# Optimization experiments

Hardware: AMD Instinct MI355X
Metric: run time of the kernel (lower is better)

Reference implementation:

```python
import jax, jax.numpy as jnp
import numpy as np

COMMITMENT_COST = 0.25


def setup_inputs() -> dict:
    key = jax.random.key(0)
    k1, k2 = jax.random.split(key)
    x = jax.random.normal(k1, (65536, 256), dtype=jnp.float32)
    codebook = jax.random.normal(k2, (1024, 256), dtype=jnp.float32)
    return {"x": x, "codebook": codebook}


def reference(x, codebook):
    # Flatten to [N, D] (already 2D here).
    flat = x.reshape(-1, codebook.shape[1])
    # Squared euclidean distances [N, K]; argmin matches torch.cdist argmin.
    x2 = jnp.sum(flat * flat, axis=1, keepdims=True)          # [N, 1]
    c2 = jnp.sum(codebook * codebook, axis=1)                  # [K]
    d2 = x2 - 2.0 * (flat @ codebook.T) + c2[None, :]          # [N, K]
    encoding_indices = jnp.argmin(d2, axis=1)                  # [N]
    quantized = codebook[encoding_indices]                     # [N, D]
    # VQ loss + commitment loss
    vq_loss = jnp.mean((jax.lax.stop_gradient(quantized) - flat) ** 2)
    commitment_loss = jnp.mean((quantized - jax.lax.stop_gradient(flat)) ** 2)
    quantization_loss = vq_loss + COMMITMENT_COST * commitment_loss
    # Straight-through estimator
    quantized_st = flat + jax.lax.stop_gradient(quantized - flat)
    quantized_st = quantized_st.reshape(x.shape)
    return quantized_st, quantization_loss, encoding_indices
```

## Files before the change

### kernel.cpp

```cpp
#include <hip/hip_runtime.h>

#define NROWS 65536
#define DDIM  256
#define KCODES 1024
#define MARGIN 0.05f
#define TIE_WINDOW 8.0e-5
#define FLAGCAP 8192

typedef __attribute__((ext_vector_type(8))) short bf16x8;
typedef __attribute__((ext_vector_type(4))) float f32x4;

union F4 { float4 v; float f[4]; };

__device__ __forceinline__ unsigned bf16rne(float f) {
    unsigned u = __float_as_uint(f);
    return (u + 0x7fffu + ((u >> 16) & 1u)) >> 16;
}
__device__ __forceinline__ float bf16tof(unsigned h) {
    return __uint_as_float(h << 16);
}

__global__ __launch_bounds__(64) void c2_kernel(const float* __restrict__ cb,
                                                float* __restrict__ c2f,
                                                double* __restrict__ c2d,
                                                int* __restrict__ cnt) {
    const int c = blockIdx.x, lane = threadIdx.x;
    if (c == 0 && lane == 0) cnt[0] = 0;
    F4 v; v.v = reinterpret_cast<const float4*>(cb + (size_t)c * DDIM)[lane];
    double s = (double)v.f[0] * v.f[0] + (double)v.f[1] * v.f[1]
             + (double)v.f[2] * v.f[2] + (double)v.f[3] * v.f[3];
    #pragma unroll
    for (int off = 32; off; off >>= 1) s += __shfl_xor(s, off);
    if (lane == 0) { c2d[c] = s; c2f[c] = (float)s; }
}

__global__ __launch_bounds__(256) void prep_frags(const float* __restrict__ cb,
                                                  unsigned short* __restrict__ fh,
                                                  unsigned short* __restrict__ fl) {
    int t = blockIdx.x * 256 + threadIdx.x;
    int j0   = (t & 1) * 4;
    int lane = (t >> 1) & 63;
    int ks   = (t >> 7) & 7;
    int ntg  = t >> 10;
    int c = ntg * 16 + (lane & 15);
    int k = ks * 32 + (lane >> 4) * 8 + j0;
    F4 v; v.v = *reinterpret_cast<const float4*>(cb + (size_t)c * DDIM + k);
    unsigned h0 = bf16rne(v.f[0]), h1 = bf16rne(v.f[1]),
             h2 = bf16rne(v.f[2]), h3 = bf16rne(v.f[3]);
    unsigned l0 = bf16rne(v.f[0] - bf16tof(h0)), l1 = bf16rne(v.f[1] - bf16tof(h1)),
             l2 = bf16rne(v.f[2] - bf16tof(h2)), l3 = bf16rne(v.f[3] - bf16tof(h3));
    unsigned* ph = reinterpret_cast<unsigned*>(fh + (size_t)t * 4);
    unsigned* pl = reinterpret_cast<unsigned*>(fl + (size_t)t * 4);
    ph[0] = h0 | (h1 << 16); ph[1] = h2 | (h3 << 16);
    pl[0] = l0 | (l1 << 16); pl[1] = l2 | (l3 << 16);
}

__global__ __launch_bounds__(512) void vqmfma(const float* __restrict__ x,
                                              const unsigned short* __restrict__ fbh,
                                              const unsigned short* __restrict__ fbl,
                                              const float* __restrict__ c2f,
                                              float* __restrict__ out_idx,
                                              int* __restrict__ flaglist,
                                              int* __restrict__ cnt,
                                              float* __restrict__ rowsq) {
    __shared__ bf16x8 lds_ah[1024];
    __shared__ bf16x8 lds_al[1024];
    __shared__ float  lds_c2[KCODES];
    __shared__ float  m_b1[256]; __shared__ float m_b2[256]; __shared__ int m_i1[256];
    __shared__ float  x2s[32];

    const int tid  = threadIdx.x;
    const int w    = tid >> 6;
    const int lane = tid & 63;
    const int row0 = blockIdx.x * 32;

    #pragma unroll
    for (int q = 0; q < 2; q++) lds_c2[q * 512 + tid] = c2f[q * 512 + tid];

    {
        const float4* gx = reinterpret_cast<const float4*>(x + (size_t)row0 * DDIM);
        unsigned* pah = reinterpret_cast<unsigned*>(lds_ah);
        unsigned* pal = reinterpret_cast<unsigned*>(lds_al);
        #pragma unroll
        for (int jj = 0; jj < 4; jj++) {
            int flat4 = jj * 512 + tid;
            int r = flat4 >> 6;
            int k = (flat4 & 63) * 4;
            F4 v; v.v = gx[flat4];
            float sq = v.f[0]*v.f[0] + v.f[1]*v.f[1] + v.f[2]*v.f[2] + v.f[3]*v.f[3];
            #pragma unroll
            for (int off = 32; off; off >>= 1) sq += __shfl_xor(sq, off);
            if (lane == 0) x2s[r] = sq;
            int rt = r >> 4, row = r & 15;
            int ks = k >> 5, gg = (k >> 3) & 3, j0 = k & 7;
            int laneS = gg * 16 + row;
            int u32i = ((((rt * 8 + ks) * 64 + laneS) * 8 + j0) >> 1);
            unsigned h0 = bf16rne(v.f[0]), h1 = bf16rne(v.f[1]),
                     h2 = bf16rne(v.f[2]), h3 = bf16rne(v.f[3]);
            pah[u32i]     = h0 | (h1 << 16);
            pah[u32i + 1] = h2 | (h3 << 16);
            unsigned l0 = bf16rne(v.f[0] - bf16tof(h0)), l1 = bf16rne(v.f[1] - bf16tof(h1)),
                     l2 = bf16rne(v.f[2] - bf16tof(h2)), l3 = bf16rne(v.f[3] - bf16tof(h3));
            pal[u32i]     = l0 | (l1 << 16);
            pal[u32i + 1] = l2 | (l3 << 16);
        }
    }
    __syncthreads();

    float bestv[8], secv[8]; int besti[8];
    #pragma unroll
    for (int e = 0; e < 8; e++) { bestv[e] = 1e30f; secv[e] = 1e30f; besti[e] = 0; }

    const bf16x8* Bh = reinterpret_cast<const bf16x8*>(fbh);
    const bf16x8* Bl = reinterpret_cast<const bf16x8*>(fbl);

    for (int cc = 0; cc < KCODES; cc += 256) {
        f32x4 acc[2][2];
        #pragma unroll
        for (int rt = 0; rt < 2; rt++)
            #pragma unroll
            for (int nt = 0; nt < 2; nt++) acc[rt][nt] = (f32x4){0.f, 0.f, 0.f, 0.f};

        const int ntg0 = (cc >> 4) + w * 2;
        const bf16x8* b0h = Bh + (size_t)(ntg0 * 8) * 64 + lane;
        const bf16x8* b0l = Bl + (size_t)(ntg0 * 8) * 64 + lane;
        const bf16x8* b1h = b0h + 8 * 64;
        const bf16x8* b1l = b0l + 8 * 64;
        const bf16x8* a0  = &lds_ah[lane];
        const bf16x8* a1  = &lds_ah[8 * 64 + lane];
        const bf16x8* a0l = &lds_al[lane];
        const bf16x8* a1l = &lds_al[8 * 64 + lane];

        #pragma unroll
        for (int ks = 0; ks < 8; ks++) {
            bf16x8 ah0 = a0[ks * 64],  ah1 = a1[ks * 64];
            bf16x8 al0 = a0l[ks * 64], al1 = a1l[ks * 64];
            bf16x8 bh0 = b0h[ks * 64], bl0 = b0l[ks * 64];
            bf16x8 bh1 = b1h[ks * 64], bl1 = b1l[ks * 64];
            acc[0][0] = __builtin_amdgcn_mfma_f32_16x16x32_bf16(ah0, bh0, acc[0][0], 0, 0, 0);
            acc[1][0] = __builtin_amdgcn_mfma_f32_16x16x32_bf16(ah1, bh0, acc[1][0], 0, 0, 0);
            acc[0][1] = __builtin_amdgcn_mfma_f32_16x16x32_bf16(ah0, bh1, acc[0][1], 0, 0, 0);
            acc[1][1] = __builtin_amdgcn_mfma_f32_16x16x32_bf16(ah1, bh1, acc[1][1], 0, 0, 0);
            acc[0][0] = __builtin_amdgcn_mfma_f32_16x16x32_bf16(ah0, bl0, acc[0][0], 0, 0, 0);
            acc[1][0] = __builtin_amdgcn_mfma_f32_16x16x32_bf16(ah1, bl0, acc[1][0], 0, 0, 0);
            acc[0][1] = __builtin_amdgcn_mfma_f32_16x16x32_bf16(ah0, bl1, acc[0][1], 0, 0, 0);
            acc[1][1] = __builtin_amdgcn_mfma_f32_16x16x32_bf16(ah1, bl1, acc[1][1], 0, 0, 0);
            acc[0][0] = __builtin_amdgcn_mfma_f32_16x16x32_bf16(al0, bh0, acc[0][0], 0, 0, 0);
            acc[1][0] = __builtin_amdgcn_mfma_f32_16x16x32_bf16(al1, bh0, acc[1][0], 0, 0, 0);
            acc[0][1] = __builtin_amdgcn_mfma_f32_16x16x32_bf16(al0, bh1, acc[0][1], 0, 0, 0);
            acc[1][1] = __builtin_amdgcn_mfma_f32_16x16x32_bf16(al1, bh1, acc[1][1], 0, 0, 0);
        }
        #pragma unroll
        for (int nt = 0; nt < 2; nt++) {
            int c = cc + w * 32 + nt * 16 + (lane & 15);
            float c2v = lds_c2[c];
            #pragma unroll
            for (int rt = 0; rt < 2; rt++)
                #pragma unroll
                for (int reg = 0; reg < 4; reg++) {
                    float s = __fmaf_rn(-2.f, acc[rt][nt][reg], c2v);
                    int e = rt * 4 + reg;
                    if (s < bestv[e]) { secv[e] = bestv[e]; bestv[e] = s; besti[e] = c; }
                    else if (s < secv[e]) secv[e] = s;
                }
        }
    }

    #pragma unroll
    for (int e = 0; e < 8; e++) {
        float b1 = bestv[e]; int i1 = besti[e]; float b2 = secv[e];
        #pragma unroll
        for (int off = 8; off; off >>= 1) {
            float o1 = __shfl_xor(b1, off, 16);
            int   oi = __shfl_xor(i1, off, 16);
            float o2 = __shfl_xor(b2, off, 16);
            if (o1 < b1 || (o1 == b1 && oi < i1)) { b2 = fminf(b1, o2); b1 = o1; i1 = oi; }
            else                                  { b2 = fminf(o1, b2); }
        }
        if ((lane & 15) == 0) {
            int rt = e >> 2, reg = e & 3;
            int rib = rt * 16 + (lane >> 4) * 4 + reg;
            m_b1[w * 32 + rib] = b1; m_i1[w * 32 + rib] = i1; m_b2[w * 32 + rib] = b2;
        }
    }
    __syncthreads();

    if (tid < 32) {
        float b1 = m_b1[tid]; int i1 = m_i1[tid]; float b2 = m_b2[tid];
        #pragma unroll
        for (int ww = 1; ww < 8; ww++) {
            float o1 = m_b1[ww * 32 + tid]; int oi = m_i1[ww * 32 + tid];
            float o2 = m_b2[ww * 32 + tid];
            if (o1 < b1 || (o1 == b1 && oi < i1)) { b2 = fminf(b1, o2); b1 = o1; i1 = oi; }
            else                                  { b2 = fminf(o1, b2); }
        }
        out_idx[row0 + tid] = (float)i1;
        rowsq[row0 + tid] = b1 + x2s[tid];
        if (b2 - b1 < MARGIN) {
            int slot = atomicAdd(cnt, 1);
            if (slot < FLAGCAP) flaglist[slot] = row0 + tid;
        }
    }
}

__global__ __launch_bounds__(256) void refine_kernel(const float* __restrict__ x,
                                                     const float* __restrict__ cb,
                                                     const double* __restrict__ c2d,
                                                     const int* __restrict__ flaglist,
                                                     const int* __restrict__ cnt,
                                                     float* __restrict__ out_idx,
                                                     float* __restrict__ rowsq) {
    __shared__ double xs[DDIM];
    __shared__ double redd[256];
    __shared__ int    redi[256];
    const int tid = threadIdx.x;
    const int n = min(cnt[0], FLAGCAP);
    for (int fi = blockIdx.x; fi < n; fi += gridDim.x) {
        const int row = flaglist[fi];
        const double xv = (double)x[(size_t)row * DDIM + tid];
        xs[tid] = xv;
        redd[tid] = xv * xv;
        __syncthreads();
        for (int off = 128; off; off >>= 1) {
            if (tid < off) redd[tid] += redd[tid + off];
            __syncthreads();
        }
        const double x2 = redd[0];
        __syncthreads();
        double d2v[4];
        #pragma unroll
        for (int j = 0; j < 4; j++) {
            const int c = tid + 256 * j;
            const float* cp = cb + (size_t)c * DDIM;
            double dot = 0.0;
            for (int d = 0; d < DDIM; d += 4) {
                F4 cv; cv.v = *reinterpret_cast<const float4*>(cp + d);
                dot += xs[d+0]*(double)cv.f[0] + xs[d+1]*(double)cv.f[1]
                     + xs[d+2]*(double)cv.f[2] + xs[d+3]*(double)cv.f[3];
            }
            d2v[j] = x2 - 2.0 * dot + c2d[c];
        }
        double mv = fmin(fmin(d2v[0], d2v[1]), fmin(d2v[2], d2v[3]));
        redd[tid] = mv;
        __syncthreads();
        for (int off = 128; off; off >>= 1) {
            if (tid < off) redd[tid] = fmin(redd[tid], redd[tid + off]);
            __syncthreads();
        }
        const double d2min = redd[0];
        const double thr = d2min + TIE_WINDOW;
        __syncthreads();
        int ci = 0x7fffffff;
        #pragma unroll
        for (int j = 0; j < 4; j++)
            if (d2v[j] <= thr) ci = min(ci, tid + 256 * j);
        redi[tid] = ci;
        __syncthreads();
        for (int off = 128; off; off >>= 1) {
            if (tid < off) redi[tid] = min(redi[tid], redi[tid + off]);
            __syncthreads();
        }
        if (tid == 0) {
            out_idx[row] = (float)redi[0];
            rowsq[row]   = (float)d2min;
        }
        __syncthreads();
    }
}

__global__ __launch_bounds__(256) void gather_slim(const float* __restrict__ cb,
                                                   const float* __restrict__ out_idx,
                                                   float* __restrict__ out_q) {
    const int tid = threadIdx.x;
    const int row = blockIdx.x * 32 + (tid >> 3);
    const int d0  = (tid & 7) * 32;
    const int bi  = (int)out_idx[row];
    const float4* gq = reinterpret_cast<const float4*>(cb + (size_t)bi * DDIM + d0);
    float4* go = reinterpret_cast<float4*>(out_q + (size_t)row * DDIM + d0);
    #pragma unroll
    for (int j = 0; j < 8; j++) go[j] = gq[j];
}

__global__ __launch_bounds__(1024) void loss_rowsq(const float* __restrict__ rowsq,
                                                   float* __restrict__ out_loss) {
    __shared__ float w[16];
    float s = 0.f;
    for (int j = threadIdx.x; j < NROWS; j += 1024) s += rowsq[j];
    #pragma unroll
    for (int off = 32; off; off >>= 1) s += __shfl_down(s, off);
    if ((threadIdx.x & 63) == 0) w[threadIdx.x >> 6] = s;
    __syncthreads();
    if (threadIdx.x == 0) {
        float tot = 0.f;
        #pragma unroll
        for (int i = 0; i < 16; i++) tot += w[i];
        out_loss[0] = 1.25f * tot / 16777216.f;
    }
}

extern "C" void kernel_launch(void* const* d_in, const int* in_sizes, int n_in,
                              void* d_out, int out_size, void* d_ws, size_t ws_size,
                              hipStream_t stream) {
    const float* x  = (const float*)d_in[0];
    const float* cb = (const float*)d_in[1];
    float* out      = (float*)d_out;
    float* out_q    = out;
    float* out_loss = out + 16777216;
    float* out_idx  = out + 16777217;

    unsigned short* fbh = (unsigned short*)d_out;
    unsigned short* fbl = fbh + 262144;

    char* wsp = (char*)d_ws;
    float*  ws_c2f   = (float*) (wsp +     0);
    double* ws_c2d   = (double*)(wsp +  4096);
    int*    ws_flag  = (int*)   (wsp + 12288);
    int*    ws_cnt   = (int*)   (wsp + 45056);
    float*  ws_rowsq = (float*) (wsp + 45120);

    c2_kernel<<<KCODES, 64, 0, stream>>>(cb, ws_c2f, ws_c2d, ws_cnt);
    prep_frags<<<256, 256, 0, stream>>>(cb, fbh, fbl);
    vqmfma<<<NROWS / 32, 512, 0, stream>>>(x, fbh, fbl, ws_c2f,
                                           out_idx, ws_flag, ws_cnt, ws_rowsq);
    refine_kernel<<<256, 256, 0, stream>>>(x, cb, ws_c2d, ws_flag, ws_cnt,
                                           out_idx, ws_rowsq);
    gather_slim<<<NROWS / 32, 256, 0, stream>>>(cb, out_idx, out_q);
    loss_rowsq<<<1, 1024, 0, stream>>>(ws_rowsq, out_loss);
}
```

Baseline: 256.4 us.

## Fuse codebook prep kernels and merge refine, gather and loss partials

```diff
diff --git a/kernel.cpp b/kernel.cpp
--- a/kernel.cpp
+++ b/kernel.cpp
@@ -5,7 +5,6 @@
 #define KCODES 1024
 #define MARGIN 0.05f
 #define TIE_WINDOW 8.0e-5
-#define FLAGCAP 8192
 
 typedef __attribute__((ext_vector_type(8))) short bf16x8;
 typedef __attribute__((ext_vector_type(4))) float f32x4;
@@ -20,37 +19,30 @@
     return __uint_as_float(h << 16);
 }
 
-__global__ __launch_bounds__(64) void c2_kernel(const float* __restrict__ cb,
-                                                float* __restrict__ c2f,
-                                                double* __restrict__ c2d,
-                                                int* __restrict__ cnt) {
+__global__ __launch_bounds__(64) void c2prep(const float* __restrict__ cb,
+                                             float* __restrict__ c2f,
+                                             double* __restrict__ c2d,
+                                             unsigned short* __restrict__ fh,
+                                             unsigned short* __restrict__ fl) {
     const int c = blockIdx.x, lane = threadIdx.x;
-    if (c == 0 && lane == 0) cnt[0] = 0;
     F4 v; v.v = reinterpret_cast<const float4*>(cb + (size_t)c * DDIM)[lane];
     double s = (double)v.f[0] * v.f[0] + (double)v.f[1] * v.f[1]
              + (double)v.f[2] * v.f[2] + (double)v.f[3] * v.f[3];
     #pragma unroll
     for (int off = 32; off; off >>= 1) s += __shfl_xor(s, off);
     if (lane == 0) { c2d[c] = s; c2f[c] = (float)s; }
-}
-
-__global__ __launch_bounds__(256) void prep_frags(const float* __restrict__ cb,
-                                                  unsigned short* __restrict__ fh,
-                                                  unsigned short* __restrict__ fl) {
-    int t = blockIdx.x * 256 + threadIdx.x;
-    int j0   = (t & 1) * 4;
-    int lane = (t >> 1) & 63;
-    int ks   = (t >> 7) & 7;
-    int ntg  = t >> 10;
-    int c = ntg * 16 + (lane & 15);
-    int k = ks * 32 + (lane >> 4) * 8 + j0;
-    F4 v; v.v = *reinterpret_cast<const float4*>(cb + (size_t)c * DDIM + k);
+
+    const int k  = lane * 4;
+    const int ks = k >> 5, g = (k >> 3) & 3, j0 = k & 7;
+    const int laneS = g * 16 + (c & 15);
+    const int ntg   = c >> 4;
+    const size_t h16 = (((size_t)(ntg * 8 + ks) * 64 + laneS) * 8 + j0);
     unsigned h0 = bf16rne(v.f[0]), h1 = bf16rne(v.f[1]),
              h2 = bf16rne(v.f[2]), h3 = bf16rne(v.f[3]);
     unsigned l0 = bf16rne(v.f[0] - bf16tof(h0)), l1 = bf16rne(v.f[1] - bf16tof(h1)),
              l2 = bf16rne(v.f[2] - bf16tof(h2)), l3 = bf16rne(v.f[3] - bf16tof(h3));
-    unsigned* ph = reinterpret_cast<unsigned*>(fh + (size_t)t * 4);
-    unsigned* pl = reinterpret_cast<unsigned*>(fl + (size_t)t * 4);
+    unsigned* ph = reinterpret_cast<unsigned*>(fh + h16);
+    unsigned* pl = reinterpret_cast<unsigned*>(fl + h16);
     ph[0] = h0 | (h1 << 16); ph[1] = h2 | (h3 << 16);
     pl[0] = l0 | (l1 << 16); pl[1] = l2 | (l3 << 16);
 }
@@ -60,8 +52,6 @@
                                               const unsigned short* __restrict__ fbl,
                                               const float* __restrict__ c2f,
                                               float* __restrict__ out_idx,
-                                              int* __restrict__ flaglist,
-                                              int* __restrict__ cnt,
                                               float* __restrict__ rowsq) {
     __shared__ bf16x8 lds_ah[1024];
     __shared__ bf16x8 lds_al[1024];
@@ -195,28 +185,36 @@
             else                                  { b2 = fminf(o1, b2); }
         }
         out_idx[row0 + tid] = (float)i1;
-        rowsq[row0 + tid] = b1 + x2s[tid];
-        if (b2 - b1 < MARGIN) {
-            int slot = atomicAdd(cnt, 1);
-            if (slot < FLAGCAP) flaglist[slot] = row0 + tid;
-        }
-    }
-}
-
-__global__ __launch_bounds__(256) void refine_kernel(const float* __restrict__ x,
-                                                     const float* __restrict__ cb,
-                                                     const double* __restrict__ c2d,
-                                                     const int* __restrict__ flaglist,
-                                                     const int* __restrict__ cnt,
-                                                     float* __restrict__ out_idx,
-                                                     float* __restrict__ rowsq) {
+        float d2b = b1 + x2s[tid];
+        rowsq[row0 + tid] = (b2 - b1 < MARGIN) ? -d2b : d2b;
+    }
+}
+
+__global__ __launch_bounds__(256) void finalize(const float* __restrict__ x,
+                                                const float* __restrict__ cb,
+                                                const double* __restrict__ c2d,
+                                                float* __restrict__ out_idx,
+                                                float* __restrict__ rowsq,
+                                                float* __restrict__ out_q,
+                                                float* __restrict__ partial) {
     __shared__ double xs[DDIM];
     __shared__ double redd[256];
     __shared__ int    redi[256];
-    const int tid = threadIdx.x;
-    const int n = min(cnt[0], FLAGCAP);
-    for (int fi = blockIdx.x; fi < n; fi += gridDim.x) {
-        const int row = flaglist[fi];
+    __shared__ int    sbest[32];
+    __shared__ float  ssq[32];
+
+    const int tid  = threadIdx.x;
+    const int row0 = blockIdx.x * 32;
+
+    if (tid < 32) {
+        sbest[tid] = (int)out_idx[row0 + tid];
+        ssq[tid]   = rowsq[row0 + tid];
+    }
+    __syncthreads();
+
+    for (int r = 0; r < 32; r++) {
+        if (!(ssq[r] < 0.f)) continue;
+        const int row = row0 + r;
         const double xv = (double)x[(size_t)row * DDIM + tid];
         xs[tid] = xv;
         redd[tid] = xv * xv;
@@ -261,41 +259,43 @@
             __syncthreads();
         }
         if (tid == 0) {
+            sbest[r] = redi[0];
+            ssq[r]   = (float)d2min;
             out_idx[row] = (float)redi[0];
-            rowsq[row]   = (float)d2min;
-        }
-        __syncthreads();
-    }
-}
-
-__global__ __launch_bounds__(256) void gather_slim(const float* __restrict__ cb,
-                                                   const float* __restrict__ out_idx,
-                                                   float* __restrict__ out_q) {
-    const int tid = threadIdx.x;
-    const int row = blockIdx.x * 32 + (tid >> 3);
-    const int d0  = (tid & 7) * 32;
-    const int bi  = (int)out_idx[row];
-    const float4* gq = reinterpret_cast<const float4*>(cb + (size_t)bi * DDIM + d0);
-    float4* go = reinterpret_cast<float4*>(out_q + (size_t)row * DDIM + d0);
-    #pragma unroll
-    for (int j = 0; j < 8; j++) go[j] = gq[j];
-}
-
-__global__ __launch_bounds__(1024) void loss_rowsq(const float* __restrict__ rowsq,
+        }
+        __syncthreads();
+    }
+    __syncthreads();
+
+    {
+        const int r  = tid >> 3;
+        const int d0 = (tid & 7) * 32;
+        const int bi = sbest[r];
+        const float4* gq = reinterpret_cast<const float4*>(cb + (size_t)bi * DDIM + d0);
+        float4* go = reinterpret_cast<float4*>(out_q + (size_t)(row0 + r) * DDIM + d0);
+        #pragma unroll
+        for (int j = 0; j < 8; j++) go[j] = gq[j];
+    }
+
+    if (tid < 32) {
+        float s = ssq[tid];
+        #pragma unroll
+        for (int off = 16; off; off >>= 1) s += __shfl_xor(s, off, 32);
+        if (tid == 0) partial[blockIdx.x] = s;
+    }
+}
+
+__global__ __launch_bounds__(256) void loss_kernel(const float* __restrict__ partial,
                                                    float* __restrict__ out_loss) {
-    __shared__ float w[16];
+    __shared__ float w[4];
     float s = 0.f;
-    for (int j = threadIdx.x; j < NROWS; j += 1024) s += rowsq[j];
+    for (int j = threadIdx.x; j < 2048; j += 256) s += partial[j];
     #pragma unroll
     for (int off = 32; off; off >>= 1) s += __shfl_down(s, off);
     if ((threadIdx.x & 63) == 0) w[threadIdx.x >> 6] = s;
     __syncthreads();
-    if (threadIdx.x == 0) {
-        float tot = 0.f;
-        #pragma unroll
-        for (int i = 0; i < 16; i++) tot += w[i];
-        out_loss[0] = 1.25f * tot / 16777216.f;
-    }
+    if (threadIdx.x == 0)
+        out_loss[0] = 1.25f * (w[0] + w[1] + w[2] + w[3]) / 16777216.f;
 }
 
 extern "C" void kernel_launch(void* const* d_in, const int* in_sizes, int n_in,
@@ -308,22 +308,18 @@
     float* out_loss = out + 16777216;
     float* out_idx  = out + 16777217;
 
-    unsigned short* fbh = (unsigned short*)d_out;
-    unsigned short* fbl = fbh + 262144;
-
     char* wsp = (char*)d_ws;
-    float*  ws_c2f   = (float*) (wsp +     0);
-    double* ws_c2d   = (double*)(wsp +  4096);
-    int*    ws_flag  = (int*)   (wsp + 12288);
-    int*    ws_cnt   = (int*)   (wsp + 45056);
-    float*  ws_rowsq = (float*) (wsp + 45120);
-
-    c2_kernel<<<KCODES, 64, 0, stream>>>(cb, ws_c2f, ws_c2d, ws_cnt);
-    prep_frags<<<256, 256, 0, stream>>>(cb, fbh, fbl);
-    vqmfma<<<NROWS / 32, 512, 0, stream>>>(x, fbh, fbl, ws_c2f,
-                                           out_idx, ws_flag, ws_cnt, ws_rowsq);
-    refine_kernel<<<256, 256, 0, stream>>>(x, cb, ws_c2d, ws_flag, ws_cnt,
+    float*  ws_c2f     = (float*) (wsp +      0);
+    double* ws_c2d     = (double*)(wsp +   4096);
+    float*  ws_rowsq   = (float*) (wsp +  12288);
+    float*  ws_partial = (float*) (wsp + 274432);
+    unsigned short* ws_fbh = (unsigned short*)(wsp + 282624);
+    unsigned short* ws_fbl = ws_fbh + 262144;
+
+    c2prep<<<KCODES, 64, 0, stream>>>(cb, ws_c2f, ws_c2d, ws_fbh, ws_fbl);
+    vqmfma<<<NROWS / 32, 512, 0, stream>>>(x, ws_fbh, ws_fbl, ws_c2f,
                                            out_idx, ws_rowsq);
-    gather_slim<<<NROWS / 32, 256, 0, stream>>>(cb, out_idx, out_q);
-    loss_rowsq<<<1, 1024, 0, stream>>>(ws_rowsq, out_loss);
-}
+    finalize<<<NROWS / 32, 256, 0, stream>>>(x, cb, ws_c2d, out_idx,
+                                             ws_rowsq, out_q, ws_partial);
+    loss_kernel<<<1, 256, 0, stream>>>(ws_partial, out_loss);
+}
```

After: 296.9 us. 15.8% more time.
